# Optimization experiments

Hardware: AMD Instinct MI355X
Metric: run time of the kernel (lower is better)

Reference implementation:

```python
import jax, jax.numpy as jnp
import numpy as np

B, L, D_MODEL = 2, 2048, 1024
EXPAND, D_STATE, D_CONV = 2, 16, 4
D_INNER = EXPAND * D_MODEL
DT_RANK = D_MODEL // 16  # mamba default: ceil(d_model/16)


def setup_inputs() -> dict:
    key = jax.random.key(0)
    ks = jax.random.split(key, 8)
    s = 0.02
    return {
        "x": jax.random.normal(ks[0], (B, L, D_MODEL), jnp.float32),
        "in_proj_w": jax.random.normal(ks[1], (2 * D_INNER, D_MODEL), jnp.float32) * s,
        "conv_w": jax.random.normal(ks[2], (D_INNER, D_CONV), jnp.float32) * s,
        "conv_b": jnp.zeros((D_INNER,), jnp.float32),
        "x_proj_w": jax.random.normal(ks[3], (DT_RANK + 2 * D_STATE, D_INNER), jnp.float32) * s,
        "dt_proj_w": jax.random.normal(ks[4], (D_INNER, DT_RANK), jnp.float32) * s,
        "dt_proj_b": jnp.full((D_INNER,), -4.6, jnp.float32),  # softplus(-4.6) ~ 0.01 dt init
        "A_log": jnp.log(jnp.broadcast_to(jnp.arange(1, D_STATE + 1, dtype=jnp.float32), (D_INNER, D_STATE))),
        "D": jnp.ones((D_INNER,), jnp.float32),
        "ssm_out_w": jax.random.normal(ks[5], (D_MODEL, D_INNER), jnp.float32) * s,
        "final_w": jax.random.normal(ks[6], (D_MODEL, D_MODEL), jnp.float32) * s,
        "final_b": jnp.zeros((D_MODEL,), jnp.float32),
    }


def _forward(x, in_proj_w, conv_w, conv_b, x_proj_w, dt_proj_w, dt_proj_b,
             A_log, D, ssm_out_w, final_w, final_b):
    d_inner, d_state = A_log.shape
    dt_rank = dt_proj_w.shape[1]
    d_conv = conv_w.shape[1]

    # in_proj -> split into x-branch and gate z  (B, L, 2*d_inner)
    xz = jnp.einsum('bld,ed->ble', x, in_proj_w)
    xin, z = jnp.split(xz, 2, axis=-1)

    # causal depthwise conv1d over time, then SiLU
    xc = jax.lax.conv_general_dilated(
        xin.swapaxes(1, 2),               # (B, d_inner, L)
        conv_w[:, None, :],               # (O=d_inner, I/g=1, W=d_conv)
        window_strides=(1,),
        padding=[(d_conv - 1, 0)],
        dimension_numbers=('NCH', 'OIH', 'NCH'),
        feature_group_count=d_inner,
    )
    xc = jax.nn.silu(xc + conv_b[None, :, None]).swapaxes(1, 2)  # (B, L, d_inner)

    # input-dependent SSM parameters
    x_dbl = jnp.einsum('bld,ed->ble', xc, x_proj_w)              # (B, L, dt_rank+2*d_state)
    dt, Bm, Cm = jnp.split(x_dbl, [dt_rank, dt_rank + d_state], axis=-1)
    delta = jax.nn.softplus(jnp.einsum('blr,dr->bld', dt, dt_proj_w) + dt_proj_b)  # (B,L,d_inner)
    A = -jnp.exp(A_log)                                          # (d_inner, d_state)

    # selective scan: h_t = exp(dt*A) h_{t-1} + dt*B_t*u_t ; y_t = <h_t, C_t>
    def step(h, t):
        delta_t, B_t, C_t, u_t = t                               # (B,Di), (B,N), (B,N), (B,Di)
        h = jnp.exp(delta_t[..., None] * A) * h + (delta_t * u_t)[..., None] * B_t[:, None, :]
        return h, jnp.einsum('bdn,bn->bd', h, C_t)

    h0 = jnp.zeros((x.shape[0], d_inner, d_state), x.dtype)
    xs = (delta.swapaxes(0, 1), Bm.swapaxes(0, 1), Cm.swapaxes(0, 1), xc.swapaxes(0, 1))
    _, ys = jax.lax.scan(step, h0, xs)                           # (L, B, d_inner)

    y = ys.swapaxes(0, 1) + xc * D                               # skip term D*u
    y = y * jax.nn.silu(z)                                       # gating
    out = jnp.einsum('bld,md->blm', y, ssm_out_w)                # Mamba out_proj -> d_model
    # wrapper: Linear(d_model, d_model) then SiLU
    return jax.nn.silu(jnp.einsum('blm,nm->bln', out, final_w) + final_b)


def reference(x, in_proj_w, conv_w, conv_b, x_proj_w, dt_proj_w, dt_proj_b,
              A_log, D, ssm_out_w, final_w, final_b):
    return _forward(x, in_proj_w, conv_w, conv_b, x_proj_w, dt_proj_w, dt_proj_b,
                    A_log, D, ssm_out_w, final_w, final_b)
```

## Files before the change

kernel.cpp:

```cpp
#include <hip/hip_runtime.h>
#include <hip/hip_bf16.h>
#include <math.h>

#define BB 2
#define LL 2048
#define DMODEL 1024
#define DINNER 2048
#define DSTATE 16
#define DCONV 4
#define DTRANK 64
#define MROWS (BB * LL)
#define XPROJ_N (DTRANK + 2 * DSTATE)

#define SEG 64
#define LS (LL / SEG)

#define XKSPLIT 8
#define XKC (DINNER / XKSPLIT)

typedef unsigned short ushort_t;
typedef short s8v __attribute__((ext_vector_type(8)));
typedef float f4v __attribute__((ext_vector_type(4)));

__device__ __forceinline__ float siluf(float x) {
    return x / (1.f + expf(-x));
}
__device__ __forceinline__ float softplusf(float x) {
    return fmaxf(x, 0.f) + log1pf(expf(-fabsf(x)));
}
__device__ __forceinline__ ushort_t f32_to_bf16(float f) {
    unsigned u = __builtin_bit_cast(unsigned, f);
    unsigned r = (u + 0x7FFFu + ((u >> 16) & 1u)) >> 16;
    return (ushort_t)r;
}
__device__ __forceinline__ float bf16_to_f32(ushort_t u) {
    return __builtin_bit_cast(float, ((unsigned)u) << 16);
}

__global__ __launch_bounds__(256) void prep_kernel(
    const float* __restrict__ x, const float* __restrict__ ipw,
    const float* __restrict__ sow, const float* __restrict__ fw,
    const float* __restrict__ xpw, const float* __restrict__ dtw,
    ushort_t* __restrict__ x_bf, ushort_t* __restrict__ ipw_bf,
    ushort_t* __restrict__ sow_bf, ushort_t* __restrict__ fw_bf,
    ushort_t* __restrict__ xpw_bf, ushort_t* __restrict__ dtw_bf,
    float4* __restrict__ xdbl_zero)
{
    const long i = ((long)blockIdx.x * 256 + threadIdx.x) * 4;
    const float* src; ushort_t* dst; long off;
    if      (i < 4194304L)  { src = x;   dst = x_bf;   off = i; }
    else if (i < 8388608L)  { src = ipw; dst = ipw_bf; off = i - 4194304L; }
    else if (i < 10485760L) { src = sow; dst = sow_bf; off = i - 8388608L; }
    else if (i < 11534336L) { src = fw;  dst = fw_bf;  off = i - 10485760L; }
    else if (i < 11730944L) { src = xpw; dst = xpw_bf; off = i - 11534336L; }
    else if (i < 11862016L) { src = dtw; dst = dtw_bf; off = i - 11730944L; }
    else { xdbl_zero[(i - 11862016L) >> 2] = make_float4(0.f, 0.f, 0.f, 0.f); return; }
    const float4 v = *reinterpret_cast<const float4*>(src + off);
    ushort_t o[4] = {f32_to_bf16(v.x), f32_to_bf16(v.y),
                     f32_to_bf16(v.z), f32_to_bf16(v.w)};
    *reinterpret_cast<uint2*>(dst + off) = *reinterpret_cast<uint2*>(o);
}

__global__ __launch_bounds__(256) void cast_dt_kernel(
    const float* __restrict__ xdbl, ushort_t* __restrict__ dtbf)
{
    const int i4 = (blockIdx.x * 256 + threadIdx.x) * 4;
    const int row = i4 >> 6;
    const int col = i4 & 63;
    const float4 v = *reinterpret_cast<const float4*>(&xdbl[(size_t)row * XPROJ_N + col]);
    ushort_t o[4] = {f32_to_bf16(v.x), f32_to_bf16(v.y),
                     f32_to_bf16(v.z), f32_to_bf16(v.w)};
    *reinterpret_cast<uint2*>(dtbf + i4) = *reinterpret_cast<uint2*>(o);
}

#define TM 128
#define TN 128
#define TBK 32

__global__ __launch_bounds__(512) void gemm_bf16_mfma(
    const ushort_t* __restrict__ A, int lda,
    const ushort_t* __restrict__ B, int ldb,
    int K,
    void* __restrict__ C0v, void* __restrict__ C1v, int splitN, int ldc,
    const float* __restrict__ bias, int act, int store_bf16)
{
    __shared__ __align__(16) ushort_t As[TM * TBK];
    __shared__ __align__(16) ushort_t Bs[TN * TBK];

    const int tid  = threadIdx.x;
    const int lane = tid & 63;
    const int w    = tid >> 6;
    const int wm   = w & 1;
    const int wn   = w >> 1;
    const int m0   = blockIdx.y * TM;
    const int n0   = blockIdx.x * TN;

    const int srow = lane >> 2;
    const int scol = (lane & 3) * 8;

    f4v acc[4][2] = {};

    for (int k0 = 0; k0 < K; k0 += TBK) {
        {
            const ushort_t* ga = A + (size_t)(m0 + w * 16 + srow) * lda + k0 + scol;
            __builtin_amdgcn_global_load_lds(
                (const __attribute__((address_space(1))) unsigned int*)ga,
                (__attribute__((address_space(3))) unsigned int*)(As + w * 512),
                16, 0, 0);
        }
        {
            const ushort_t* gb = B + (size_t)(n0 + w * 16 + srow) * ldb + k0 + scol;
            __builtin_amdgcn_global_load_lds(
                (const __attribute__((address_space(1))) unsigned int*)gb,
                (__attribute__((address_space(3))) unsigned int*)(Bs + w * 512),
                16, 0, 0);
        }
        __syncthreads();

        const int fr = lane & 15;
        const int kg = lane >> 4;
        s8v a[4], b[2];
        #pragma unroll
        for (int t = 0; t < 4; ++t)
            a[t] = *reinterpret_cast<const s8v*>(As + (wm * 64 + t * 16 + fr) * TBK + kg * 8);
        #pragma unroll
        for (int t = 0; t < 2; ++t)
            b[t] = *reinterpret_cast<const s8v*>(Bs + (wn * 32 + t * 16 + fr) * TBK + kg * 8);
        #pragma unroll
        for (int i = 0; i < 4; ++i)
            #pragma unroll
            for (int j = 0; j < 2; ++j)
                acc[i][j] = __builtin_amdgcn_mfma_f32_16x16x32_bf16(
                    a[i], b[j], acc[i][j], 0, 0, 0);
        __syncthreads();
    }

    const int rbase = (lane >> 4) * 4;
    const int cbase = lane & 15;
    #pragma unroll
    for (int i = 0; i < 4; ++i) {
        #pragma unroll
        for (int j = 0; j < 2; ++j) {
            const int row = m0 + wm * 64 + i * 16 + rbase;
            const int col = n0 + wn * 32 + j * 16 + cbase;
            void* Cp = C0v;
            int c2 = col;
            if (C1v && col >= splitN) { Cp = C1v; c2 = col - splitN; }
            const float bv = bias ? bias[col] : 0.f;
            #pragma unroll
            for (int r = 0; r < 4; ++r) {
                float v = acc[i][j][r] + bv;
                if (act == 1) v = siluf(v);
                else if (act == 2) v = softplusf(v);
                if (store_bf16)
                    ((ushort_t*)Cp)[(size_t)(row + r) * ldc + c2] = f32_to_bf16(v);
                else
                    ((float*)Cp)[(size_t)(row + r) * ldc + c2] = v;
            }
        }
    }
}

__global__ __launch_bounds__(256) void xproj_mfma(
    const ushort_t* __restrict__ A, const ushort_t* __restrict__ Bw,
    float* __restrict__ Cout)
{
    __shared__ __align__(16) ushort_t As[64 * 32];
    __shared__ __align__(16) ushort_t Bs[96 * 32];

    const int tid = threadIdx.x;
    const int lane = tid & 63;
    const int w = tid >> 6;
    const int kbase = blockIdx.x * XKC;
    const int m0 = blockIdx.y * 64;

    const int srow = lane >> 2;
    const int scol = (lane & 3) * 8;

    f4v acc[6] = {};

    for (int k0 = kbase; k0 < kbase + XKC; k0 += 32) {
        {
            const ushort_t* ga = A + (size_t)(m0 + w * 16 + srow) * DINNER + k0 + scol;
            __builtin_amdgcn_global_load_lds(
                (const __attribute__((address_space(1))) unsigned int*)ga,
                (__attribute__((address_space(3))) unsigned int*)(As + (w * 16) * 32),
                16, 0, 0);
        }
        {
            const ushort_t* gb = Bw + (size_t)(w * 16 + srow) * DINNER + k0 + scol;
            __builtin_amdgcn_global_load_lds(
                (const __attribute__((address_space(1))) unsigned int*)gb,
                (__attribute__((address_space(3))) unsigned int*)(Bs + (w * 16) * 32),
                16, 0, 0);
        }
        if (w < 2) {
            const ushort_t* gb = Bw + (size_t)((4 + w) * 16 + srow) * DINNER + k0 + scol;
            __builtin_amdgcn_global_load_lds(
                (const __attribute__((address_space(1))) unsigned int*)gb,
                (__attribute__((address_space(3))) unsigned int*)(Bs + ((4 + w) * 16) * 32),
                16, 0, 0);
        }
        __syncthreads();

        const int fr = lane & 15;
        const int kg = lane >> 4;
        const s8v a = *reinterpret_cast<const s8v*>(As + (w * 16 + fr) * 32 + kg * 8);
        #pragma unroll
        for (int j = 0; j < 6; ++j) {
            const s8v b = *reinterpret_cast<const s8v*>(Bs + (j * 16 + fr) * 32 + kg * 8);
            acc[j] = __builtin_amdgcn_mfma_f32_16x16x32_bf16(a, b, acc[j], 0, 0, 0);
        }
        __syncthreads();
    }

    const int rbase = (lane >> 4) * 4;
    const int cb = lane & 15;
    #pragma unroll
    for (int j = 0; j < 6; ++j)
        #pragma unroll
        for (int r = 0; r < 4; ++r)
            atomicAdd(&Cout[(size_t)(m0 + w * 16 + rbase + r) * XPROJ_N + j * 16 + cb],
                      acc[j][r]);
}

__global__ __launch_bounds__(256) void conv_silu_kernel(
    const ushort_t* __restrict__ xin, const float* __restrict__ w,
    const float* __restrict__ b, ushort_t* __restrict__ xcbf)
{
    const int idx = blockIdx.x * blockDim.x + threadIdx.x;
    const int c = idx % DINNER;
    const int bl = idx / DINNER;
    const int l = bl % LL;
    const int bb = bl / LL;
    if (bb >= BB) return;

    const ushort_t* xp = xin + (size_t)bb * LL * DINNER + c;
    float acc = b[c];
    #pragma unroll
    for (int k = 0; k < DCONV; ++k) {
        const int ll = l - (DCONV - 1) + k;
        if (ll >= 0)
            acc = fmaf(bf16_to_f32(xp[(size_t)ll * DINNER]), w[c * DCONV + k], acc);
    }
    xcbf[idx] = f32_to_bf16(siluf(acc));
}

__global__ __launch_bounds__(256) void scan_part1(
    const ushort_t* __restrict__ delta, const float* __restrict__ xdbl,
    const ushort_t* __restrict__ xc, const float* __restrict__ A_log,
    float* __restrict__ hloc, float* __restrict__ decay)
{
    const int d = blockIdx.x * 256 + threadIdx.x;
    const int seg = blockIdx.y;
    const int b = blockIdx.z;
    const int t0 = seg * LS;

    float Ad[DSTATE];
    #pragma unroll
    for (int n = 0; n < DSTATE; ++n)
        Ad[n] = -expf(A_log[d * DSTATE + n]);

    float h[DSTATE];
    #pragma unroll
    for (int n = 0; n < DSTATE; ++n) h[n] = 0.f;

    const ushort_t* dp = delta + ((size_t)b * LL) * DINNER + d;
    const ushort_t* up = xc    + ((size_t)b * LL) * DINNER + d;
    const float*    xb = xdbl  + ((size_t)b * LL) * XPROJ_N;

    float sum_dl = 0.f;
    for (int t = t0; t < t0 + LS; ++t) {
        const float dl = bf16_to_f32(dp[(size_t)t * DINNER]);
        const float u  = bf16_to_f32(up[(size_t)t * DINNER]);
        const float4 b0 = *reinterpret_cast<const float4*>(&xb[t * XPROJ_N + DTRANK + 0]);
        const float4 b1 = *reinterpret_cast<const float4*>(&xb[t * XPROJ_N + DTRANK + 4]);
        const float4 b2 = *reinterpret_cast<const float4*>(&xb[t * XPROJ_N + DTRANK + 8]);
        const float4 b3 = *reinterpret_cast<const float4*>(&xb[t * XPROJ_N + DTRANK + 12]);
        const float Bv[DSTATE] = {b0.x, b0.y, b0.z, b0.w, b1.x, b1.y, b1.z, b1.w,
                                  b2.x, b2.y, b2.z, b2.w, b3.x, b3.y, b3.z, b3.w};
        const float dlu = dl * u;
        sum_dl += dl;
        #pragma unroll
        for (int n = 0; n < DSTATE; ++n)
            h[n] = __expf(dl * Ad[n]) * h[n] + dlu * Bv[n];
    }

    const size_t base = (((size_t)b * SEG + seg) * DSTATE) * DINNER + d;
    #pragma unroll
    for (int n = 0; n < DSTATE; ++n) {
        hloc[base + (size_t)n * DINNER]  = h[n];
        decay[base + (size_t)n * DINNER] = __expf(Ad[n] * sum_dl);
    }
}

__global__ __launch_bounds__(256) void scan_combine(
    float* __restrict__ hloc, const float* __restrict__ decay)
{
    const int idx = blockIdx.x * 256 + threadIdx.x;
    const int d = idx % DINNER;
    const int n = (idx / DINNER) % DSTATE;
    const int b = idx / (DINNER * DSTATE);
    if (b >= BB) return;

    float carry = 0.f;
    for (int s = 0; s < SEG; ++s) {
        const size_t off = (((size_t)b * SEG + s) * DSTATE + n) * DINNER + d;
        const float hl = hloc[off];
        hloc[off] = carry;
        carry = decay[off] * carry + hl;
    }
}

__global__ __launch_bounds__(256) void scan_part2(
    const ushort_t* __restrict__ delta, const float* __restrict__ xdbl,
    const ushort_t* __restrict__ xc, const ushort_t* __restrict__ z,
    const float* __restrict__ A_log, const float* __restrict__ Dvec,
    const float* __restrict__ hstart, ushort_t* __restrict__ ybf)
{
    const int d = blockIdx.x * 256 + threadIdx.x;
    const int seg = blockIdx.y;
    const int b = blockIdx.z;
    const int t0 = seg * LS;

    float Ad[DSTATE];
    #pragma unroll
    for (int n = 0; n < DSTATE; ++n)
        Ad[n] = -expf(A_log[d * DSTATE + n]);

    float h[DSTATE];
    const size_t hbase = (((size_t)b * SEG + seg) * DSTATE) * DINNER + d;
    #pragma unroll
    for (int n = 0; n < DSTATE; ++n)
        h[n] = hstart[hbase + (size_t)n * DINNER];

    const float Dd = Dvec[d];
    const ushort_t* dp = delta + ((size_t)b * LL) * DINNER + d;
    const ushort_t* up = xc    + ((size_t)b * LL) * DINNER + d;
    const float*    xb = xdbl  + ((size_t)b * LL) * XPROJ_N;
    const ushort_t* zp = z     + ((size_t)b * LL) * DINNER + d;
    ushort_t*       yp = ybf   + ((size_t)b * LL) * DINNER + d;

    for (int t = t0; t < t0 + LS; ++t) {
        const float dl = bf16_to_f32(dp[(size_t)t * DINNER]);
        const float u  = bf16_to_f32(up[(size_t)t * DINNER]);
        const float zv = bf16_to_f32(zp[(size_t)t * DINNER]);
        const float4 b0 = *reinterpret_cast<const float4*>(&xb[t * XPROJ_N + DTRANK + 0]);
        const float4 b1 = *reinterpret_cast<const float4*>(&xb[t * XPROJ_N + DTRANK + 4]);
        const float4 b2 = *reinterpret_cast<const float4*>(&xb[t * XPROJ_N + DTRANK + 8]);
        const float4 b3 = *reinterpret_cast<const float4*>(&xb[t * XPROJ_N + DTRANK + 12]);
        const float4 c0 = *reinterpret_cast<const float4*>(&xb[t * XPROJ_N + DTRANK + DSTATE + 0]);
        const float4 c1 = *reinterpret_cast<const float4*>(&xb[t * XPROJ_N + DTRANK + DSTATE + 4]);
        const float4 c2 = *reinterpret_cast<const float4*>(&xb[t * XPROJ_N + DTRANK + DSTATE + 8]);
        const float4 c3 = *reinterpret_cast<const float4*>(&xb[t * XPROJ_N + DTRANK + DSTATE + 12]);
        const float Bv[DSTATE] = {b0.x, b0.y, b0.z, b0.w, b1.x, b1.y, b1.z, b1.w,
                                  b2.x, b2.y, b2.z, b2.w, b3.x, b3.y, b3.z, b3.w};
        const float Cv[DSTATE] = {c0.x, c0.y, c0.z, c0.w, c1.x, c1.y, c1.z, c1.w,
                                  c2.x, c2.y, c2.z, c2.w, c3.x, c3.y, c3.z, c3.w};
        const float dlu = dl * u;
        float y = 0.f;
        #pragma unroll
        for (int n = 0; n < DSTATE; ++n) {
            h[n] = __expf(dl * Ad[n]) * h[n] + dlu * Bv[n];
            y = fmaf(h[n], Cv[n], y);
        }
        yp[(size_t)t * DINNER] = f32_to_bf16((y + u * Dd) * siluf(zv));
    }
}

extern "C" void kernel_launch(void* const* d_in, const int* in_sizes, int n_in,
                              void* d_out, int out_size, void* d_ws, size_t ws_size,
                              hipStream_t stream) {
    const float* x         = (const float*)d_in[0];
    const float* in_proj_w = (const float*)d_in[1];
    const float* conv_w    = (const float*)d_in[2];
    const float* conv_b    = (const float*)d_in[3];
    const float* x_proj_w  = (const float*)d_in[4];
    const float* dt_proj_w = (const float*)d_in[5];
    const float* dt_proj_b = (const float*)d_in[6];
    const float* A_log     = (const float*)d_in[7];
    const float* Dvec      = (const float*)d_in[8];
    const float* ssm_out_w = (const float*)d_in[9];
    const float* final_w   = (const float*)d_in[10];
    const float* final_b   = (const float*)d_in[11];
    float* out = (float*)d_out;

    const size_t MB = 1024 * 1024;
    char* base = (char*)d_ws;
    ushort_t* xin_bf   = (ushort_t*)(base);
    ushort_t* z_bf     = (ushort_t*)(base + 16 * MB);
    ushort_t* xc_bf    = (ushort_t*)(base + 32 * MB);
    ushort_t* delta_bf = (ushort_t*)(base + 48 * MB);
    float*    xdbl     = (float*)(base + 64 * MB);
    ushort_t* x_bf     = (ushort_t*)(base + 78 * MB);
    ushort_t* ipw_bf   = (ushort_t*)(base + 86 * MB);
    ushort_t* sow_bf   = (ushort_t*)(base + 94 * MB);
    ushort_t* fw_bf    = (ushort_t*)(base + 98 * MB);
    ushort_t* xpw_bf   = (ushort_t*)(base + 100 * MB);
    ushort_t* dtw_bf   = (ushort_t*)(base + 100 * MB + 512 * 1024);
    ushort_t* dt_bf    = (ushort_t*)(base + 101 * MB);
    ushort_t* y_bf     = (ushort_t*)(base + 102 * MB);
    ushort_t* outb_bf  = (ushort_t*)(base + 118 * MB);
    float* hloc  = (float*)(base);
    float* decay = (float*)(base + 78 * MB);

    prep_kernel<<<11968, 256, 0, stream>>>(
        x, in_proj_w, ssm_out_w, final_w, x_proj_w, dt_proj_w,
        x_bf, ipw_bf, sow_bf, fw_bf, xpw_bf, dtw_bf, (float4*)xdbl);

    gemm_bf16_mfma<<<dim3(2 * DINNER / TN, MROWS / TM), 512, 0, stream>>>(
        x_bf, DMODEL, ipw_bf, DMODEL, DMODEL,
        xin_bf, z_bf, DINNER, DINNER, nullptr, 0, 1);

    conv_silu_kernel<<<(MROWS * DINNER) / 256, 256, 0, stream>>>(
        xin_bf, conv_w, conv_b, xc_bf);

    xproj_mfma<<<dim3(XKSPLIT, MROWS / 64), 256, 0, stream>>>(xc_bf, xpw_bf, xdbl);

    cast_dt_kernel<<<(MROWS * DTRANK / 4) / 256, 256, 0, stream>>>(xdbl, dt_bf);
    gemm_bf16_mfma<<<dim3(DINNER / TN, MROWS / TM), 512, 0, stream>>>(
        dt_bf, DTRANK, dtw_bf, DTRANK, DTRANK,
        delta_bf, nullptr, 1 << 30, DINNER, dt_proj_b, 2, 1);

    scan_part1<<<dim3(DINNER / 256, SEG, BB), 256, 0, stream>>>(
        delta_bf, xdbl, xc_bf, A_log, hloc, decay);
    scan_combine<<<(BB * DSTATE * DINNER) / 256, 256, 0, stream>>>(hloc, decay);
    scan_part2<<<dim3(DINNER / 256, SEG, BB), 256, 0, stream>>>(
        delta_bf, xdbl, xc_bf, z_bf, A_log, Dvec, hloc, y_bf);

    gemm_bf16_mfma<<<dim3(DMODEL / TN, MROWS / TM), 512, 0, stream>>>(
        y_bf, DINNER, sow_bf, DINNER, DINNER,
        outb_bf, nullptr, 1 << 30, DMODEL, nullptr, 0, 1);

    gemm_bf16_mfma<<<dim3(DMODEL / TN, MROWS / TM), 512, 0, stream>>>(
        outb_bf, DMODEL, fw_bf, DMODEL, DMODEL,
        out, nullptr, 1 << 30, DMODEL, final_b, 1, 0);
}
```

Measured before the change: 395.9 us.

## Split scan state across 4 lanes and add smaller-tile GEMM for narrow outputs

The scan kernels now assign four threads per channel, each holding four of the sixteen state elements, and combine the output with two lane shuffles. This cuts per-thread registers and gives the scan four times as many threads. A new 64x128-tile MFMA GEMM replaces the larger-tile GEMM for the dt projection and the two d_model-wide projections, which yields more blocks on these small-N matrices. The costs are redundant loads of delta, u and z in each lane of a group, shuffle overhead, and less data reuse per block in the GEMMs.

```diff
diff --git a/kernel.cpp b/kernel.cpp
--- a/kernel.cpp
+++ b/kernel.cpp
@@ -14,6 +14,7 @@
 
 #define SEG 64
 #define LS (LL / SEG)
+#define DPB 64
 
 #define XKSPLIT 8
 #define XKC (DINNER / XKSPLIT)
@@ -161,6 +162,90 @@
     }
 }
 
+#define UM 64
+#define UN 128
+
+__global__ __launch_bounds__(512) void gemm64_bf16_mfma(
+    const ushort_t* __restrict__ A, int lda,
+    const ushort_t* __restrict__ B, int ldb,
+    int K,
+    void* __restrict__ C0v, int ldc,
+    const float* __restrict__ bias, int act, int store_bf16)
+{
+    __shared__ __align__(16) ushort_t As[UM * TBK];
+    __shared__ __align__(16) ushort_t Bs[UN * TBK];
+
+    const int tid  = threadIdx.x;
+    const int lane = tid & 63;
+    const int w    = tid >> 6;
+    const int wm   = w & 1;
+    const int wn   = w >> 1;
+    const int m0   = blockIdx.y * UM;
+    const int n0   = blockIdx.x * UN;
+
+    const int srow = lane >> 2;
+    const int scol = (lane & 3) * 8;
+
+    f4v acc[2][2] = {};
+
+    for (int k0 = 0; k0 < K; k0 += TBK) {
+        if (w < 4) {
+            const ushort_t* ga = A + (size_t)(m0 + w * 16 + srow) * lda + k0 + scol;
+            __builtin_amdgcn_global_load_lds(
+                (const __attribute__((address_space(1))) unsigned int*)ga,
+                (__attribute__((address_space(3))) unsigned int*)(As + w * 512),
+                16, 0, 0);
+        }
+        {
+            const ushort_t* gb = B + (size_t)(n0 + w * 16 + srow) * ldb + k0 + scol;
+            __builtin_amdgcn_global_load_lds(
+                (const __attribute__((address_space(1))) unsigned int*)gb,
+                (__attribute__((address_space(3))) unsigned int*)(Bs + w * 512),
+                16, 0, 0);
+        }
+        __syncthreads();
+
+        const int fr = lane & 15;
+        const int kg = lane >> 4;
+        s8v a[2], b[2];
+        #pragma unroll
+        for (int t = 0; t < 2; ++t)
+            a[t] = *reinterpret_cast<const s8v*>(As + (wm * 32 + t * 16 + fr) * TBK + kg * 8);
+        #pragma unroll
+        for (int t = 0; t < 2; ++t)
+            b[t] = *reinterpret_cast<const s8v*>(Bs + (wn * 32 + t * 16 + fr) * TBK + kg * 8);
+        #pragma unroll
+        for (int i = 0; i < 2; ++i)
+            #pragma unroll
+            for (int j = 0; j < 2; ++j)
+                acc[i][j] = __builtin_amdgcn_mfma_f32_16x16x32_bf16(
+                    a[i], b[j], acc[i][j], 0, 0, 0);
+        __syncthreads();
+    }
+
+    const int rbase = (lane >> 4) * 4;
+    const int cbase = lane & 15;
+    #pragma unroll
+    for (int i = 0; i < 2; ++i) {
+        #pragma unroll
+        for (int j = 0; j < 2; ++j) {
+            const int row = m0 + wm * 32 + i * 16 + rbase;
+            const int col = n0 + wn * 32 + j * 16 + cbase;
+            const float bv = bias ? bias[col] : 0.f;
+            #pragma unroll
+            for (int r = 0; r < 4; ++r) {
+                float v = acc[i][j][r] + bv;
+                if (act == 1) v = siluf(v);
+                else if (act == 2) v = softplusf(v);
+                if (store_bf16)
+                    ((ushort_t*)C0v)[(size_t)(row + r) * ldc + col] = f32_to_bf16(v);
+                else
+                    ((float*)C0v)[(size_t)(row + r) * ldc + col] = v;
+            }
+        }
+    }
+}
+
 __global__ __launch_bounds__(256) void xproj_mfma(
     const ushort_t* __restrict__ A, const ushort_t* __restrict__ Bw,
     float* __restrict__ Cout)
@@ -251,19 +336,19 @@
     const ushort_t* __restrict__ xc, const float* __restrict__ A_log,
     float* __restrict__ hloc, float* __restrict__ decay)
 {
-    const int d = blockIdx.x * 256 + threadIdx.x;
+    const int tid = threadIdx.x;
+    const int nsub = tid & 3;
+    const int d = blockIdx.x * DPB + (tid >> 2);
     const int seg = blockIdx.y;
     const int b = blockIdx.z;
     const int t0 = seg * LS;
 
-    float Ad[DSTATE];
-    #pragma unroll
-    for (int n = 0; n < DSTATE; ++n)
-        Ad[n] = -expf(A_log[d * DSTATE + n]);
-
-    float h[DSTATE];
-    #pragma unroll
-    for (int n = 0; n < DSTATE; ++n) h[n] = 0.f;
+    float Ad[4];
+    #pragma unroll
+    for (int i = 0; i < 4; ++i)
+        Ad[i] = -expf(A_log[d * DSTATE + nsub * 4 + i]);
+
+    float h[4] = {};
 
     const ushort_t* dp = delta + ((size_t)b * LL) * DINNER + d;
     const ushort_t* up = xc    + ((size_t)b * LL) * DINNER + d;
@@ -273,24 +358,21 @@
     for (int t = t0; t < t0 + LS; ++t) {
         const float dl = bf16_to_f32(dp[(size_t)t * DINNER]);
         const float u  = bf16_to_f32(up[(size_t)t * DINNER]);
-        const float4 b0 = *reinterpret_cast<const float4*>(&xb[t * XPROJ_N + DTRANK + 0]);
-        const float4 b1 = *reinterpret_cast<const float4*>(&xb[t * XPROJ_N + DTRANK + 4]);
-        const float4 b2 = *reinterpret_cast<const float4*>(&xb[t * XPROJ_N + DTRANK + 8]);
-        const float4 b3 = *reinterpret_cast<const float4*>(&xb[t * XPROJ_N + DTRANK + 12]);
-        const float Bv[DSTATE] = {b0.x, b0.y, b0.z, b0.w, b1.x, b1.y, b1.z, b1.w,
-                                  b2.x, b2.y, b2.z, b2.w, b3.x, b3.y, b3.z, b3.w};
+        const float4 Bv = *reinterpret_cast<const float4*>(
+            &xb[t * XPROJ_N + DTRANK + nsub * 4]);
+        const float bv[4] = {Bv.x, Bv.y, Bv.z, Bv.w};
         const float dlu = dl * u;
         sum_dl += dl;
         #pragma unroll
-        for (int n = 0; n < DSTATE; ++n)
-            h[n] = __expf(dl * Ad[n]) * h[n] + dlu * Bv[n];
-    }
-
-    const size_t base = (((size_t)b * SEG + seg) * DSTATE) * DINNER + d;
-    #pragma unroll
-    for (int n = 0; n < DSTATE; ++n) {
-        hloc[base + (size_t)n * DINNER]  = h[n];
-        decay[base + (size_t)n * DINNER] = __expf(Ad[n] * sum_dl);
+        for (int i = 0; i < 4; ++i)
+            h[i] = __expf(dl * Ad[i]) * h[i] + dlu * bv[i];
+    }
+
+    const size_t base = (((size_t)b * SEG + seg) * DSTATE + nsub * 4) * DINNER + d;
+    #pragma unroll
+    for (int i = 0; i < 4; ++i) {
+        hloc[base + (size_t)i * DINNER]  = h[i];
+        decay[base + (size_t)i * DINNER] = __expf(Ad[i] * sum_dl);
     }
 }
 
@@ -318,21 +400,23 @@
     const float* __restrict__ A_log, const float* __restrict__ Dvec,
     const float* __restrict__ hstart, ushort_t* __restrict__ ybf)
 {
-    const int d = blockIdx.x * 256 + threadIdx.x;
+    const int tid = threadIdx.x;
+    const int nsub = tid & 3;
+    const int d = blockIdx.x * DPB + (tid >> 2);
     const int seg = blockIdx.y;
     const int b = blockIdx.z;
     const int t0 = seg * LS;
 
-    float Ad[DSTATE];
-    #pragma unroll
-    for (int n = 0; n < DSTATE; ++n)
-        Ad[n] = -expf(A_log[d * DSTATE + n]);
-
-    float h[DSTATE];
-    const size_t hbase = (((size_t)b * SEG + seg) * DSTATE) * DINNER + d;
-    #pragma unroll
-    for (int n = 0; n < DSTATE; ++n)
-        h[n] = hstart[hbase + (size_t)n * DINNER];
+    float Ad[4];
+    #pragma unroll
+    for (int i = 0; i < 4; ++i)
+        Ad[i] = -expf(A_log[d * DSTATE + nsub * 4 + i]);
+
+    float h[4];
+    const size_t hbase = (((size_t)b * SEG + seg) * DSTATE + nsub * 4) * DINNER + d;
+    #pragma unroll
+    for (int i = 0; i < 4; ++i)
+        h[i] = hstart[hbase + (size_t)i * DINNER];
 
     const float Dd = Dvec[d];
     const ushort_t* dp = delta + ((size_t)b * LL) * DINNER + d;
@@ -345,26 +429,23 @@
         const float dl = bf16_to_f32(dp[(size_t)t * DINNER]);
         const float u  = bf16_to_f32(up[(size_t)t * DINNER]);
         const float zv = bf16_to_f32(zp[(size_t)t * DINNER]);
-        const float4 b0 = *reinterpret_cast<const float4*>(&xb[t * XPROJ_N + DTRANK + 0]);
-        const float4 b1 = *reinterpret_cast<const float4*>(&xb[t * XPROJ_N + DTRANK + 4]);
-        const float4 b2 = *reinterpret_cast<const float4*>(&xb[t * XPROJ_N + DTRANK + 8]);
-        const float4 b3 = *reinterpret_cast<const float4*>(&xb[t * XPROJ_N + DTRANK + 12]);
-        const float4 c0 = *reinterpret_cast<const float4*>(&xb[t * XPROJ_N + DTRANK + DSTATE + 0]);
-        const float4 c1 = *reinterpret_cast<const float4*>(&xb[t * XPROJ_N + DTRANK + DSTATE + 4]);
-        const float4 c2 = *reinterpret_cast<const float4*>(&xb[t * XPROJ_N + DTRANK + DSTATE + 8]);
-        const float4 c3 = *reinterpret_cast<const float4*>(&xb[t * XPROJ_N + DTRANK + DSTATE + 12]);
-        const float Bv[DSTATE] = {b0.x, b0.y, b0.z, b0.w, b1.x, b1.y, b1.z, b1.w,
-                                  b2.x, b2.y, b2.z, b2.w, b3.x, b3.y, b3.z, b3.w};
-        const float Cv[DSTATE] = {c0.x, c0.y, c0.z, c0.w, c1.x, c1.y, c1.z, c1.w,
-                                  c2.x, c2.y, c2.z, c2.w, c3.x, c3.y, c3.z, c3.w};
+        const float4 Bv = *reinterpret_cast<const float4*>(
+            &xb[t * XPROJ_N + DTRANK + nsub * 4]);
+        const float4 Cv = *reinterpret_cast<const float4*>(
+            &xb[t * XPROJ_N + DTRANK + DSTATE + nsub * 4]);
+        const float bv[4] = {Bv.x, Bv.y, Bv.z, Bv.w};
+        const float cv[4] = {Cv.x, Cv.y, Cv.z, Cv.w};
         const float dlu = dl * u;
         float y = 0.f;
         #pragma unroll
-        for (int n = 0; n < DSTATE; ++n) {
-            h[n] = __expf(dl * Ad[n]) * h[n] + dlu * Bv[n];
-            y = fmaf(h[n], Cv[n], y);
-        }
-        yp[(size_t)t * DINNER] = f32_to_bf16((y + u * Dd) * siluf(zv));
+        for (int i = 0; i < 4; ++i) {
+            h[i] = __expf(dl * Ad[i]) * h[i] + dlu * bv[i];
+            y = fmaf(h[i], cv[i], y);
+        }
+        y += __shfl_xor(y, 1);
+        y += __shfl_xor(y, 2);
+        if (nsub == 0)
+            yp[(size_t)t * DINNER] = f32_to_bf16((y + u * Dd) * siluf(zv));
     }
 }
 
@@ -418,21 +499,21 @@
     xproj_mfma<<<dim3(XKSPLIT, MROWS / 64), 256, 0, stream>>>(xc_bf, xpw_bf, xdbl);
 
     cast_dt_kernel<<<(MROWS * DTRANK / 4) / 256, 256, 0, stream>>>(xdbl, dt_bf);
-    gemm_bf16_mfma<<<dim3(DINNER / TN, MROWS / TM), 512, 0, stream>>>(
+    gemm64_bf16_mfma<<<dim3(DINNER / UN, MROWS / UM), 512, 0, stream>>>(
         dt_bf, DTRANK, dtw_bf, DTRANK, DTRANK,
-        delta_bf, nullptr, 1 << 30, DINNER, dt_proj_b, 2, 1);
-
-    scan_part1<<<dim3(DINNER / 256, SEG, BB), 256, 0, stream>>>(
+        delta_bf, DINNER, dt_proj_b, 2, 1);
+
+    scan_part1<<<dim3(DINNER / DPB, SEG, BB), 256, 0, stream>>>(
         delta_bf, xdbl, xc_bf, A_log, hloc, decay);
     scan_combine<<<(BB * DSTATE * DINNER) / 256, 256, 0, stream>>>(hloc, decay);
-    scan_part2<<<dim3(DINNER / 256, SEG, BB), 256, 0, stream>>>(
+    scan_part2<<<dim3(DINNER / DPB, SEG, BB), 256, 0, stream>>>(
         delta_bf, xdbl, xc_bf, z_bf, A_log, Dvec, hloc, y_bf);
 
-    gemm_bf16_mfma<<<dim3(DMODEL / TN, MROWS / TM), 512, 0, stream>>>(
+    gemm64_bf16_mfma<<<dim3(DMODEL / UN, MROWS / UM), 512, 0, stream>>>(
         y_bf, DINNER, sow_bf, DINNER, DINNER,
-        outb_bf, nullptr, 1 << 30, DMODEL, nullptr, 0, 1);
-
-    gemm_bf16_mfma<<<dim3(DMODEL / TN, MROWS / TM), 512, 0, stream>>>(
+        outb_bf, DMODEL, nullptr, 0, 1);
+
+    gemm64_bf16_mfma<<<dim3(DMODEL / UN, MROWS / UM), 512, 0, stream>>>(
         outb_bf, DMODEL, fw_bf, DMODEL, DMODEL,
-        out, nullptr, 1 << 30, DMODEL, final_b, 1, 0);
-}
+        out, DMODEL, final_b, 1, 0);
+}
```

After: 417.7 us. 5.5% more time.
